# Optimization experiments

Measured on AMD Instinct MI355X. Metric: run time of the kernel, lower is better.

Reference implementation:

```python
import jax, jax.numpy as jnp
import numpy as np

N = 200000   # nodes
DEG = 32     # fixed padded degree
B = 16384    # batch of target nodes
D = 128      # feature dim (app/loc/time)
H = 128      # hidden dim
L = 5        # walk length (hard-coded in original forward)


def setup_inputs() -> dict:
    key = jax.random.key(0)
    ks = jax.random.split(key, 12)
    return {
        "x_app": jax.random.normal(ks[0], (N, D), jnp.float32),
        "x_loc": jax.random.normal(ks[1], (N, D), jnp.float32),
        "x_time": jax.random.normal(ks[2], (N, H), jnp.float32),
        "neighbors": jax.random.randint(ks[3], (N, DEG), 0, N, jnp.int32),
        "edge_weight": jax.random.uniform(ks[4], (N, DEG), jnp.float32, 1e-4, 1.0),
        "target_nodes": jax.random.randint(ks[5], (B,), 0, N, jnp.int32),
        "W_app": 0.05 * jax.random.normal(ks[6], (2 * D, H), jnp.float32),
        "b_app": jnp.zeros((H,), jnp.float32),
        "W_loc": 0.05 * jax.random.normal(ks[7], (2 * D, H), jnp.float32),
        "b_loc": jnp.zeros((H,), jnp.float32),
        "W_att": 0.05 * jax.random.normal(ks[8], (D + H, 1), jnp.float32),
        "b_att": jnp.zeros((1,), jnp.float32),
    }


def _walks(neighbors, edge_weight, start, key):
    """Batched weighted random walk. start: [B] -> walk node ids [B, L+1]."""
    def step(cur, k):
        nbrs = neighbors[cur]                 # [B, DEG] gather
        w = edge_weight[cur]                  # [B, DEG]
        # multinomial(prob,1) == categorical over log-weights
        c = jax.random.categorical(k, jnp.log(w), axis=-1)   # [B]
        nxt = jnp.take_along_axis(nbrs, c[:, None], axis=1)[:, 0]
        return nxt, nxt
    _, steps = jax.lax.scan(step, start, jax.random.split(key, L))  # steps: [L, B]
    return jnp.concatenate([start[None, :], steps], axis=0).T       # [B, L+1]


def reference(x_app, x_loc, x_time, neighbors, edge_weight, target_nodes,
              W_app, b_app, W_loc, b_loc, W_att, b_att):
    kw = jax.random.key(42)
    k1, k2 = jax.random.split(kw)
    app_walk = _walks(neighbors, edge_weight, target_nodes, k1)  # [B, L+1]
    loc_walk = _walks(neighbors, edge_weight, target_nodes, k2)  # [B, L+1]

    t_app = x_app[target_nodes]                                   # [B, D]
    t_loc = x_loc[target_nodes]                                   # [B, D]

    # SameTypeAggregator: sum neighbor feats, cat with target, Linear+ReLU
    f_app = jax.nn.relu(jnp.concatenate([t_app, x_app[app_walk].sum(axis=1)], axis=-1) @ W_app + b_app)
    f_loc = jax.nn.relu(jnp.concatenate([t_loc, x_loc[loc_walk].sum(axis=1)], axis=-1) @ W_loc + b_loc)

    # CrossTypeAttention over 3 feature types
    feats = jnp.stack([f_app, f_loc, x_time[target_nodes]], axis=0)      # [3, B, H]
    tgt = jnp.broadcast_to(t_app[None], (3,) + t_app.shape)              # [3, B, D]
    combined = jnp.concatenate([tgt, feats], axis=-1)                    # [3, B, D+H]
    scores = jax.nn.softmax(combined @ W_att + b_att, axis=0)            # [3, B, 1]
    return (scores * feats).sum(axis=0)                                  # [B, H]
```

## Files before the change

### kernel.cpp

```cpp
#include <hip/hip_runtime.h>
#include <stdint.h>

#define NN 200000
#define DEG 32
#define BB 16384
#define DD 128
#define HH 128
#define BM 16

typedef __attribute__((ext_vector_type(8))) short bf16x8;
typedef __attribute__((ext_vector_type(4))) float f32x4;

struct Keys { unsigned a[5][2]; unsigned l[5][2]; };

__host__ __device__ __forceinline__ unsigned rotl32(unsigned v, int r) {
  return (v << r) | (v >> (32 - r));
}

__host__ __device__ __forceinline__ void threefry2x32(
    unsigned k0, unsigned k1, unsigned x0, unsigned x1,
    unsigned* o0, unsigned* o1) {
  unsigned ks0 = k0, ks1 = k1, ks2 = k0 ^ k1 ^ 0x1BD11BDAu;
  x0 += ks0; x1 += ks1;
#define TF_RND(r) { x0 += x1; x1 = rotl32(x1, (r)); x1 ^= x0; }
  TF_RND(13) TF_RND(15) TF_RND(26) TF_RND(6)
  x0 += ks1; x1 += ks2 + 1u;
  TF_RND(17) TF_RND(29) TF_RND(16) TF_RND(24)
  x0 += ks2; x1 += ks0 + 2u;
  TF_RND(13) TF_RND(15) TF_RND(26) TF_RND(6)
  x0 += ks0; x1 += ks1 + 3u;
  TF_RND(17) TF_RND(29) TF_RND(16) TF_RND(24)
  x0 += ks1; x1 += ks2 + 4u;
  TF_RND(13) TF_RND(15) TF_RND(26) TF_RND(6)
  x0 += ks2; x1 += ks0 + 5u;
#undef TF_RND
  *o0 = x0; *o1 = x1;
}

__device__ __forceinline__ unsigned short f2bf(float x) {
  unsigned u = __float_as_uint(x);
  unsigned r = (u + 0x7fffu + ((u >> 16) & 1u)) >> 16;
  return (unsigned short)r;
}

__global__ __launch_bounds__(256) void walk_kernel(
    const int* __restrict__ neighbors, const float* __restrict__ ew,
    const int* __restrict__ target, int* __restrict__ walks, Keys keys) {
  int lane = threadIdx.x & 63;
  int sub = lane & 31;
  int grp = (int)((blockIdx.x * 256 + threadIdx.x) >> 5);
  int wk = grp >= BB ? 1 : 0;
  int b = grp - wk * BB;

  int cur = target[b];
  if (sub == 0) walks[(size_t)grp * 6] = cur;

  const float TINY = 1.17549435e-38f;

  for (int s = 0; s < 5; ++s) {
    int nb = neighbors[(size_t)cur * DEG + sub];
    float w = ew[(size_t)cur * DEG + sub];
    unsigned j = (unsigned)b * DEG + (unsigned)sub;
    unsigned k0 = wk ? keys.l[s][0] : keys.a[s][0];
    unsigned k1 = wk ? keys.l[s][1] : keys.a[s][1];
    unsigned y0, y1;
    threefry2x32(k0, k1, 0u, j, &y0, &y1);
    unsigned bits = y0 ^ y1;
    float f = __uint_as_float((bits >> 9) | 0x3f800000u) - 1.0f;
    float u = fmaxf(TINY, f + TINY);
    float g = -logf(-logf(u));
    float v = g + logf(w);
    int idx = sub;
    #pragma unroll
    for (int off = 16; off; off >>= 1) {
      float vo = __shfl_xor(v, off);
      int io = __shfl_xor(idx, off);
      if (vo > v || (vo == v && io < idx)) { v = vo; idx = io; }
    }
    cur = __shfl(nb, (lane & 32) + idx);
    if (sub == 0) walks[(size_t)grp * 6 + s + 1] = cur;
  }
}

__global__ __launch_bounds__(256) void prep_w(
    const float* __restrict__ Wapp, const float* __restrict__ Wloc,
    unsigned short* __restrict__ Wt) {
  int blk = blockIdx.x;
  int mat = blk >> 3;
  int k0 = (blk & 7) << 5;
  const float* W = mat ? Wloc : Wapp;
  __shared__ float tile[32][129];
  int t = threadIdx.x;
  #pragma unroll
  for (int i = 0; i < 16; ++i) {
    int idx = t + (i << 8);
    int kk = idx >> 7, n = idx & 127;
    tile[kk][n] = W[((size_t)(k0 + kk) << 7) + n];
  }
  __syncthreads();
  int n = t >> 1, h = (t & 1) << 4;
  unsigned pk[8];
  #pragma unroll
  for (int j = 0; j < 8; ++j) {
    float lo = tile[h + 2 * j][n];
    float hi = tile[h + 2 * j + 1][n];
    pk[j] = (unsigned)f2bf(lo) | ((unsigned)f2bf(hi) << 16);
  }
  unsigned short* dst = Wt + ((size_t)mat << 15) + ((size_t)n << 8) + k0 + h;
  uint4 lo4; lo4.x = pk[0]; lo4.y = pk[1]; lo4.z = pk[2]; lo4.w = pk[3];
  uint4 hi4; hi4.x = pk[4]; hi4.y = pk[5]; hi4.z = pk[6]; hi4.w = pk[7];
  reinterpret_cast<uint4*>(dst)[0] = lo4;
  reinterpret_cast<uint4*>(dst)[1] = hi4;
}

__global__ __launch_bounds__(256, 4) void fuse3(
    const float* __restrict__ x_app, const float* __restrict__ x_loc,
    const float* __restrict__ x_time, const int* __restrict__ target,
    const int* __restrict__ walks, const unsigned short* __restrict__ Wt,
    const float* __restrict__ W_att, const float* __restrict__ b_att,
    const float* __restrict__ b_app, const float* __restrict__ b_loc,
    float* __restrict__ out) {
  __shared__ unsigned short sA[BM][264];
  __shared__ unsigned short sL[BM][264];
  __shared__ float attT[BM];
  __shared__ float4 sRed[4][BM];

  int tid = threadIdx.x;
  int b0 = blockIdx.x * BM;
  int hw = tid >> 5;
  int c = tid & 31;

  #pragma unroll
  for (int it = 0; it < BM / 8; ++it) {
    int row = (it << 3) + hw;
    {
      const int* wp = walks + (size_t)(b0 + row) * 6;
      int n0 = wp[0], n1 = wp[1], n2 = wp[2], n3 = wp[3], n4 = wp[4], n5 = wp[5];
      const float4 v0 = *(const float4*)&x_app[((size_t)n0 << 7) + 4 * c];
      const float4 v1 = *(const float4*)&x_app[((size_t)n1 << 7) + 4 * c];
      const float4 v2 = *(const float4*)&x_app[((size_t)n2 << 7) + 4 * c];
      const float4 v3 = *(const float4*)&x_app[((size_t)n3 << 7) + 4 * c];
      const float4 v4 = *(const float4*)&x_app[((size_t)n4 << 7) + 4 * c];
      const float4 v5 = *(const float4*)&x_app[((size_t)n5 << 7) + 4 * c];
      float sx = v0.x + v1.x + v2.x + v3.x + v4.x + v5.x;
      float sy = v0.y + v1.y + v2.y + v3.y + v4.y + v5.y;
      float sz = v0.z + v1.z + v2.z + v3.z + v4.z + v5.z;
      float sw = v0.w + v1.w + v2.w + v3.w + v4.w + v5.w;
      uint2 pt, ps;
      pt.x = (unsigned)f2bf(v0.x) | ((unsigned)f2bf(v0.y) << 16);
      pt.y = (unsigned)f2bf(v0.z) | ((unsigned)f2bf(v0.w) << 16);
      ps.x = (unsigned)f2bf(sx) | ((unsigned)f2bf(sy) << 16);
      ps.y = (unsigned)f2bf(sz) | ((unsigned)f2bf(sw) << 16);
      *(uint2*)&sA[row][4 * c] = pt;
      *(uint2*)&sA[row][128 + 4 * c] = ps;
      const float4 wa = *(const float4*)&W_att[4 * c];
      float p = v0.x * wa.x + v0.y * wa.y + v0.z * wa.z + v0.w * wa.w;
      #pragma unroll
      for (int off = 16; off; off >>= 1) p += __shfl_xor(p, off);
      if (c == 0) attT[row] = p;
    }
    {
      const int* wp = walks + (size_t)(BB + b0 + row) * 6;
      int n0 = wp[0], n1 = wp[1], n2 = wp[2], n3 = wp[3], n4 = wp[4], n5 = wp[5];
      const float4 v0 = *(const float4*)&x_loc[((size_t)n0 << 7) + 4 * c];
      const float4 v1 = *(const float4*)&x_loc[((size_t)n1 << 7) + 4 * c];
      const float4 v2 = *(const float4*)&x_loc[((size_t)n2 << 7) + 4 * c];
      const float4 v3 = *(const float4*)&x_loc[((size_t)n3 << 7) + 4 * c];
      const float4 v4 = *(const float4*)&x_loc[((size_t)n4 << 7) + 4 * c];
      const float4 v5 = *(const float4*)&x_loc[((size_t)n5 << 7) + 4 * c];
      float sx = v0.x + v1.x + v2.x + v3.x + v4.x + v5.x;
      float sy = v0.y + v1.y + v2.y + v3.y + v4.y + v5.y;
      float sz = v0.z + v1.z + v2.z + v3.z + v4.z + v5.z;
      float sw = v0.w + v1.w + v2.w + v3.w + v4.w + v5.w;
      uint2 pt, ps;
      pt.x = (unsigned)f2bf(v0.x) | ((unsigned)f2bf(v0.y) << 16);
      pt.y = (unsigned)f2bf(v0.z) | ((unsigned)f2bf(v0.w) << 16);
      ps.x = (unsigned)f2bf(sx) | ((unsigned)f2bf(sy) << 16);
      ps.y = (unsigned)f2bf(sz) | ((unsigned)f2bf(sw) << 16);
      *(uint2*)&sL[row][4 * c] = pt;
      *(uint2*)&sL[row][128 + 4 * c] = ps;
    }
  }
  __syncthreads();

  int w = tid >> 6;
  int l = tid & 63;
  int r15 = l & 15, g = l >> 4;

  f32x4 accA[2], accL[2];
  {
    bf16x8 aF[8], lF[8];
    #pragma unroll
    for (int k = 0; k < 8; ++k) {
      aF[k] = *(const bf16x8*)&sA[r15][(k << 5) + (g << 3)];
      lF[k] = *(const bf16x8*)&sL[r15][(k << 5) + (g << 3)];
    }
    #pragma unroll
    for (int n = 0; n < 2; ++n) {
      int col = ((w << 1) + n) << 4;
      f32x4 a1 = {0.f, 0.f, 0.f, 0.f}, a2 = {0.f, 0.f, 0.f, 0.f};
      #pragma unroll
      for (int k = 0; k < 8; ++k) {
        bf16x8 bA = *(const bf16x8*)&Wt[(((size_t)col + r15) << 8) + (k << 5) + (g << 3)];
        bf16x8 bL = *(const bf16x8*)&Wt[(1 << 15) + (((size_t)col + r15) << 8) + (k << 5) + (g << 3)];
        a1 = __builtin_amdgcn_mfma_f32_16x16x32_bf16(aF[k], bA, a1, 0, 0, 0);
        a2 = __builtin_amdgcn_mfma_f32_16x16x32_bf16(lF[k], bL, a2, 0, 0, 0);
      }
      accA[n] = a1;
      accL[n] = a2;
    }
  }

  float bA[2], bL[2], wv[2];
  #pragma unroll
  for (int n = 0; n < 2; ++n) {
    int col = (((w << 1) + n) << 4) + r15;
    bA[n] = b_app[col];
    bL[n] = b_loc[col];
    wv[n] = W_att[128 + col];
  }
  float batt = b_att[0];

  int trow[4];
  #pragma unroll
  for (int r = 0; r < 4; ++r) trow[r] = target[b0 + (g << 2) + r];
  float tts[2][4];
  #pragma unroll
  for (int n = 0; n < 2; ++n)
    #pragma unroll
    for (int r = 0; r < 4; ++r)
      tts[n][r] = x_time[((size_t)trow[r] << 7) + (((w << 1) + n) << 4) + r15];

  float fa[2][4], fl[2][4];
  #pragma unroll
  for (int r = 0; r < 4; ++r) {
    float dA = 0.f, dL = 0.f, dT = 0.f;
    #pragma unroll
    for (int n = 0; n < 2; ++n) {
      fa[n][r] = fmaxf(accA[n][r] + bA[n], 0.f);
      fl[n][r] = fmaxf(accL[n][r] + bL[n], 0.f);
      dA += fa[n][r] * wv[n];
      dL += fl[n][r] * wv[n];
      dT += tts[n][r] * wv[n];
    }
    #pragma unroll
    for (int off = 1; off < 16; off <<= 1) {
      dA += __shfl_xor(dA, off);
      dL += __shfl_xor(dL, off);
      dT += __shfl_xor(dT, off);
    }
    if (r15 == 0) {
      float4 q; q.x = dA; q.y = dL; q.z = dT; q.w = 0.f;
      sRed[w][(g << 2) + r] = q;
    }
  }
  __syncthreads();

  #pragma unroll
  for (int r = 0; r < 4; ++r) {
    int row = (g << 2) + r;
    float4 q0 = sRed[0][row], q1 = sRed[1][row], q2 = sRed[2][row], q3 = sRed[3][row];
    float at = attT[row] + batt;
    float s0 = at + q0.x + q1.x + q2.x + q3.x;
    float s1 = at + q0.y + q1.y + q2.y + q3.y;
    float s2 = at + q0.z + q1.z + q2.z + q3.z;
    float m = fmaxf(s0, fmaxf(s1, s2));
    float e0 = expf(s0 - m), e1 = expf(s1 - m), e2 = expf(s2 - m);
    float inv = 1.f / (e0 + e1 + e2);
    size_t grow = (size_t)(b0 + row);
    #pragma unroll
    for (int n = 0; n < 2; ++n) {
      int col = (((w << 1) + n) << 4) + r15;
      out[(grow << 7) + col] = (e0 * fa[n][r] + e1 * fl[n][r] + e2 * tts[n][r]) * inv;
    }
  }
}

extern "C" void kernel_launch(void* const* d_in, const int* in_sizes, int n_in,
                              void* d_out, int out_size, void* d_ws, size_t ws_size,
                              hipStream_t stream) {
  (void)in_sizes; (void)n_in; (void)out_size; (void)ws_size;
  const float* x_app   = (const float*)d_in[0];
  const float* x_loc   = (const float*)d_in[1];
  const float* x_time  = (const float*)d_in[2];
  const int*   neighbors = (const int*)d_in[3];
  const float* ew      = (const float*)d_in[4];
  const int*   target  = (const int*)d_in[5];
  const float* W_app   = (const float*)d_in[6];
  const float* b_app   = (const float*)d_in[7];
  const float* W_loc   = (const float*)d_in[8];
  const float* b_loc   = (const float*)d_in[9];
  const float* W_att   = (const float*)d_in[10];
  const float* b_att   = (const float*)d_in[11];
  float* out = (float*)d_out;
  int* walks = (int*)d_ws;
  unsigned short* Wt =
      (unsigned short*)((char*)d_ws + (size_t)2 * BB * 6 * sizeof(int));

  Keys keys;
  unsigned k1a, k1b, k2a, k2b;
  threefry2x32(0u, 42u, 0u, 0u, &k1a, &k1b);
  threefry2x32(0u, 42u, 0u, 1u, &k2a, &k2b);
  for (unsigned s = 0; s < 5; ++s) {
    threefry2x32(k1a, k1b, 0u, s, &keys.a[s][0], &keys.a[s][1]);
    threefry2x32(k2a, k2b, 0u, s, &keys.l[s][0], &keys.l[s][1]);
  }

  walk_kernel<<<(2 * BB * 32) / 256, 256, 0, stream>>>(neighbors, ew, target, walks, keys);
  prep_w<<<16, 256, 0, stream>>>(W_app, W_loc, Wt);
  fuse3<<<BB / BM, 256, 0, stream>>>(x_app, x_loc, x_time, target, walks, Wt,
                                     W_att, b_att, b_app, b_loc, out);
}
```

Baseline: 61.13 us.

## Fuse random-walk generation into the aggregation kernel and stage walks in LDS

Removes the separate walk kernel and computes both weighted random walks inside the main fused kernel, with each half-wave handling four walk units and keeping node ids in shared memory instead of a global workspace. The x_time row is now loaded during the gather phase into shared memory, coalesced, rather than by scattered per-lane loads later. The app and loc MFMA loops are split so fewer fragments are live at once, and occupancy is lowered to 2 blocks per SM. This drops a kernel launch and the global round trip of walk ids. In exchange, the serial walk latency now sits inside every block ahead of the gathers, and LDS use per block grows.

```diff
diff --git a/kernel.cpp b/kernel.cpp
--- a/kernel.cpp
+++ b/kernel.cpp
@@ -43,45 +43,6 @@
   return (unsigned short)r;
 }
 
-__global__ __launch_bounds__(256) void walk_kernel(
-    const int* __restrict__ neighbors, const float* __restrict__ ew,
-    const int* __restrict__ target, int* __restrict__ walks, Keys keys) {
-  int lane = threadIdx.x & 63;
-  int sub = lane & 31;
-  int grp = (int)((blockIdx.x * 256 + threadIdx.x) >> 5);
-  int wk = grp >= BB ? 1 : 0;
-  int b = grp - wk * BB;
-
-  int cur = target[b];
-  if (sub == 0) walks[(size_t)grp * 6] = cur;
-
-  const float TINY = 1.17549435e-38f;
-
-  for (int s = 0; s < 5; ++s) {
-    int nb = neighbors[(size_t)cur * DEG + sub];
-    float w = ew[(size_t)cur * DEG + sub];
-    unsigned j = (unsigned)b * DEG + (unsigned)sub;
-    unsigned k0 = wk ? keys.l[s][0] : keys.a[s][0];
-    unsigned k1 = wk ? keys.l[s][1] : keys.a[s][1];
-    unsigned y0, y1;
-    threefry2x32(k0, k1, 0u, j, &y0, &y1);
-    unsigned bits = y0 ^ y1;
-    float f = __uint_as_float((bits >> 9) | 0x3f800000u) - 1.0f;
-    float u = fmaxf(TINY, f + TINY);
-    float g = -logf(-logf(u));
-    float v = g + logf(w);
-    int idx = sub;
-    #pragma unroll
-    for (int off = 16; off; off >>= 1) {
-      float vo = __shfl_xor(v, off);
-      int io = __shfl_xor(idx, off);
-      if (vo > v || (vo == v && io < idx)) { v = vo; idx = io; }
-    }
-    cur = __shfl(nb, (lane & 32) + idx);
-    if (sub == 0) walks[(size_t)grp * 6 + s + 1] = cur;
-  }
-}
-
 __global__ __launch_bounds__(256) void prep_w(
     const float* __restrict__ Wapp, const float* __restrict__ Wloc,
     unsigned short* __restrict__ Wt) {
@@ -113,35 +74,76 @@
   reinterpret_cast<uint4*>(dst)[1] = hi4;
 }
 
-__global__ __launch_bounds__(256, 4) void fuse3(
+__global__ __launch_bounds__(256, 2) void fuse8(
     const float* __restrict__ x_app, const float* __restrict__ x_loc,
-    const float* __restrict__ x_time, const int* __restrict__ target,
-    const int* __restrict__ walks, const unsigned short* __restrict__ Wt,
+    const float* __restrict__ x_time, const int* __restrict__ neighbors,
+    const float* __restrict__ ew, const int* __restrict__ target,
+    const unsigned short* __restrict__ Wt,
     const float* __restrict__ W_att, const float* __restrict__ b_att,
     const float* __restrict__ b_app, const float* __restrict__ b_loc,
-    float* __restrict__ out) {
+    float* __restrict__ out, Keys keys) {
   __shared__ unsigned short sA[BM][264];
   __shared__ unsigned short sL[BM][264];
+  __shared__ float sT[BM][128];
+  __shared__ int wn[2][BM][6];
   __shared__ float attT[BM];
   __shared__ float4 sRed[4][BM];
 
   int tid = threadIdx.x;
   int b0 = blockIdx.x * BM;
-  int hw = tid >> 5;
-  int c = tid & 31;
-
+  int lane = tid & 63;
+  int sub = lane & 31;
+  int hw_g = tid >> 5;
+
+  const float TINY = 1.17549435e-38f;
+
+  for (int u = 0; u < 4; ++u) {
+    int unit = (hw_g << 2) + u;
+    int side = unit >> 4;
+    int t = unit & 15;
+    int b = b0 + t;
+    int cur = target[b];
+    if (sub == 0) wn[side][t][0] = cur;
+    for (int s = 0; s < 5; ++s) {
+      int nb = neighbors[(size_t)cur * DEG + sub];
+      float w = ew[(size_t)cur * DEG + sub];
+      unsigned j = (unsigned)b * DEG + (unsigned)sub;
+      unsigned k0 = side ? keys.l[s][0] : keys.a[s][0];
+      unsigned k1 = side ? keys.l[s][1] : keys.a[s][1];
+      unsigned y0, y1;
+      threefry2x32(k0, k1, 0u, j, &y0, &y1);
+      unsigned bits = y0 ^ y1;
+      float f = __uint_as_float((bits >> 9) | 0x3f800000u) - 1.0f;
+      float uu = fmaxf(TINY, f + TINY);
+      float gg = -logf(-logf(uu));
+      float v = gg + logf(w);
+      int idx = sub;
+      #pragma unroll
+      for (int off = 16; off; off >>= 1) {
+        float vo = __shfl_xor(v, off);
+        int io = __shfl_xor(idx, off);
+        if (vo > v || (vo == v && io < idx)) { v = vo; idx = io; }
+      }
+      cur = __shfl(nb, (lane & 32) + idx);
+      if (sub == 0) wn[side][t][s + 1] = cur;
+    }
+  }
+  __syncthreads();
+
+  int c = sub;
   #pragma unroll
   for (int it = 0; it < BM / 8; ++it) {
-    int row = (it << 3) + hw;
+    int row = (it << 3) + hw_g;
     {
-      const int* wp = walks + (size_t)(b0 + row) * 6;
-      int n0 = wp[0], n1 = wp[1], n2 = wp[2], n3 = wp[3], n4 = wp[4], n5 = wp[5];
+      int n0 = wn[0][row][0], n1 = wn[0][row][1], n2 = wn[0][row][2];
+      int n3 = wn[0][row][3], n4 = wn[0][row][4], n5 = wn[0][row][5];
       const float4 v0 = *(const float4*)&x_app[((size_t)n0 << 7) + 4 * c];
       const float4 v1 = *(const float4*)&x_app[((size_t)n1 << 7) + 4 * c];
       const float4 v2 = *(const float4*)&x_app[((size_t)n2 << 7) + 4 * c];
       const float4 v3 = *(const float4*)&x_app[((size_t)n3 << 7) + 4 * c];
       const float4 v4 = *(const float4*)&x_app[((size_t)n4 << 7) + 4 * c];
       const float4 v5 = *(const float4*)&x_app[((size_t)n5 << 7) + 4 * c];
+      const float4 tv = *(const float4*)&x_time[((size_t)n0 << 7) + 4 * c];
       float sx = v0.x + v1.x + v2.x + v3.x + v4.x + v5.x;
       float sy = v0.y + v1.y + v2.y + v3.y + v4.y + v5.y;
       float sz = v0.z + v1.z + v2.z + v3.z + v4.z + v5.z;
@@ -153,6 +155,7 @@
       ps.y = (unsigned)f2bf(sz) | ((unsigned)f2bf(sw) << 16);
       *(uint2*)&sA[row][4 * c] = pt;
       *(uint2*)&sA[row][128 + 4 * c] = ps;
+      *(float4*)&sT[row][4 * c] = tv;
       const float4 wa = *(const float4*)&W_att[4 * c];
       float p = v0.x * wa.x + v0.y * wa.y + v0.z * wa.z + v0.w * wa.w;
       #pragma unroll
@@ -160,8 +163,8 @@
       if (c == 0) attT[row] = p;
     }
     {
-      const int* wp = walks + (size_t)(BB + b0 + row) * 6;
-      int n0 = wp[0], n1 = wp[1], n2 = wp[2], n3 = wp[3], n4 = wp[4], n5 = wp[5];
+      int n0 = wn[1][row][0], n1 = wn[1][row][1], n2 = wn[1][row][2];
+      int n3 = wn[1][row][3], n4 = wn[1][row][4], n5 = wn[1][row][5];
       const float4 v0 = *(const float4*)&x_loc[((size_t)n0 << 7) + 4 * c];
       const float4 v1 = *(const float4*)&x_loc[((size_t)n1 << 7) + 4 * c];
       const float4 v2 = *(const float4*)&x_loc[((size_t)n2 << 7) + 4 * c];
@@ -189,25 +192,38 @@
 
   f32x4 accA[2], accL[2];
   {
-    bf16x8 aF[8], lF[8];
-    #pragma unroll
-    for (int k = 0; k < 8; ++k) {
+    bf16x8 aF[8];
+    #pragma unroll
+    for (int k = 0; k < 8; ++k)
       aF[k] = *(const bf16x8*)&sA[r15][(k << 5) + (g << 3)];
-      lF[k] = *(const bf16x8*)&sL[r15][(k << 5) + (g << 3)];
-    }
     #pragma unroll
     for (int n = 0; n < 2; ++n) {
-      int col = ((w << 1) + n) << 4;
-      f32x4 a1 = {0.f, 0.f, 0.f, 0.f}, a2 = {0.f, 0.f, 0.f, 0.f};
+      size_t colBase = ((size_t)((((w << 1) + n) << 4) + r15)) << 8;
+      f32x4 acc = {0.f, 0.f, 0.f, 0.f};
       #pragma unroll
       for (int k = 0; k < 8; ++k) {
-        bf16x8 bA = *(const bf16x8*)&Wt[(((size_t)col + r15) << 8) + (k << 5) + (g << 3)];
-        bf16x8 bL = *(const bf16x8*)&Wt[(1 << 15) + (((size_t)col + r15) << 8) + (k << 5) + (g << 3)];
-        a1 = __builtin_amdgcn_mfma_f32_16x16x32_bf16(aF[k], bA, a1, 0, 0, 0);
-        a2 = __builtin_amdgcn_mfma_f32_16x16x32_bf16(lF[k], bL, a2, 0, 0, 0);
+        bf16x8 bF = *(const bf16x8*)&Wt[colBase + (k << 5) + (g << 3)];
+        acc = __builtin_amdgcn_mfma_f32_16x16x32_bf16(aF[k], bF, acc, 0, 0, 0);
       }
-      accA[n] = a1;
-      accL[n] = a2;
+      accA[n] = acc;
+    }
+  }
+  {
+    bf16x8 lF[8];
+    #pragma unroll
+    for (int k = 0; k < 8; ++k)
+      lF[k] = *(const bf16x8*)&sL[r15][(k << 5) + (g << 3)];
+    const unsigned short* WtL = Wt + (1 << 15);
+    #pragma unroll
+    for (int n = 0; n < 2; ++n) {
+      size_t colBase = ((size_t)((((w << 1) + n) << 4) + r15)) << 8;
+      f32x4 acc = {0.f, 0.f, 0.f, 0.f};
+      #pragma unroll
+      for (int k = 0; k < 8; ++k) {
+        bf16x8 bF = *(const bf16x8*)&WtL[colBase + (k << 5) + (g << 3)];
+        acc = __builtin_amdgcn_mfma_f32_16x16x32_bf16(lF[k], bF, acc, 0, 0, 0);
+      }
+      accL[n] = acc;
     }
   }
 
@@ -221,15 +237,12 @@
   }
   float batt = b_att[0];
 
-  int trow[4];
-  #pragma unroll
-  for (int r = 0; r < 4; ++r) trow[r] = target[b0 + (g << 2) + r];
   float tts[2][4];
   #pragma unroll
   for (int n = 0; n < 2; ++n)
     #pragma unroll
     for (int r = 0; r < 4; ++r)
-      tts[n][r] = x_time[((size_t)trow[r] << 7) + (((w << 1) + n) << 4) + r15];
+      tts[n][r] = sT[(g << 2) + r][(((w << 1) + n) << 4) + r15];
 
   float fa[2][4], fl[2][4];
   #pragma unroll
@@ -293,9 +306,7 @@
   const float* W_att   = (const float*)d_in[10];
   const float* b_att   = (const float*)d_in[11];
   float* out = (float*)d_out;
-  int* walks = (int*)d_ws;
-  unsigned short* Wt =
-      (unsigned short*)((char*)d_ws + (size_t)2 * BB * 6 * sizeof(int));
+  unsigned short* Wt = (unsigned short*)d_ws;
 
   Keys keys;
   unsigned k1a, k1b, k2a, k2b;
@@ -306,8 +317,8 @@
     threefry2x32(k2a, k2b, 0u, s, &keys.l[s][0], &keys.l[s][1]);
   }
 
-  walk_kernel<<<(2 * BB * 32) / 256, 256, 0, stream>>>(neighbors, ew, target, walks, keys);
   prep_w<<<16, 256, 0, stream>>>(W_app, W_loc, Wt);
-  fuse3<<<BB / BM, 256, 0, stream>>>(x_app, x_loc, x_time, target, walks, Wt,
-                                     W_att, b_att, b_app, b_loc, out);
-}
+  fuse8<<<BB / BM, 256, 0, stream>>>(x_app, x_loc, x_time, neighbors, ew,
+                                     target, Wt, W_att, b_att, b_app, b_loc,
+                                     out, keys);
+}
```

Result: faster. 56.64 us (-7.4%).
